# Kernel tuning notes

Hardware: AMD Instinct MI355X
Metric: run time of the kernel (lower is better)

Reference implementation:

```python
import jax, jax.numpy as jnp
import numpy as np

EPS = 1e-12  # F.normalize default eps


def _l2norm(x, axis):
    n = jnp.sqrt(jnp.sum(x * x, axis=axis, keepdims=True))
    return x / jnp.maximum(n, EPS)


def setup_inputs() -> dict:
    key = jax.random.key(0)
    k1, k2, k3, k4 = jax.random.split(key, 4)
    N, T, C, K = 64, 577, 768, 64
    return {
        "grids": jax.random.normal(k1, (N, T, C), dtype=jnp.float32),
        "conv_w": jax.random.normal(k2, (K, C), dtype=jnp.float32) * 0.03,
        "conv_b": jax.random.normal(k3, (K,), dtype=jnp.float32) * 0.01,
        "centroids": jax.random.normal(k4, (K, C), dtype=jnp.float32) * 0.03,
    }


def reference(grids, conv_w, conv_b, centroids):
    # grids: (N, 577, 768) -> (N, C=768, T=577), matching view+permute in torch
    N = grids.shape[0]
    x = jnp.transpose(grids.reshape(N, 577, 768), (0, 2, 1))  # (N, C, T)
    # per-token L2 normalization over channel dim
    x = _l2norm(x, axis=1)
    # 1x1 conv == per-token linear: (N, K, T)
    logits = jnp.einsum('kc,nct->nkt', conv_w, x) + conv_b[None, :, None]
    a = jax.nn.softmax(logits, axis=1)  # softmax over regions K
    # NetVLAD algebraic rewrite of sum_t a[n,k,t]*(x[n,:,t]-c[k,:]):
    #   = (a @ x^T)[n,k,c] - sum_t(a)[n,k] * c[k,c]
    p = jnp.einsum('nkt,nct->nkc', a, x) - a.sum(axis=-1)[:, :, None] * centroids[None]
    p = _l2norm(p, axis=2)             # intra-region normalization
    p = p.reshape(N, -1)               # (N, K*C)
    p = _l2norm(p, axis=1)             # global normalization
    return p
```

## Files before the change

kernel.cpp:

```cpp
#include <hip/hip_runtime.h>
#include <math.h>

#define TT 577
#define TP 640
#define CCH 768
#define KR 64
#define NB 64

typedef __attribute__((ext_vector_type(8))) short bf16x8;
typedef __attribute__((ext_vector_type(8))) unsigned short ushort8;
typedef __attribute__((ext_vector_type(4))) float f32x4;

static constexpr float EPSF = 1e-12f;

static __device__ inline unsigned short f2bf(float f) {
    union { float f; unsigned int u; } v; v.f = f;
    return (unsigned short)((v.u + 0x7FFFu + ((v.u >> 16) & 1u)) >> 16);
}

__global__ __launch_bounds__(256) void k_logits(
    const float* __restrict__ grids,
    const float* __restrict__ conv_w,
    const float* __restrict__ conv_b,
    unsigned short* __restrict__ ws_a,
    float* __restrict__ ws_asum)
{
    __shared__ __align__(16) unsigned short Wl[2][KR * 136];

    const int tid  = threadIdx.x;
    const int lane = tid & 63;
    const int w    = tid >> 6;
    const int n    = blockIdx.x / 10;
    const int tb   = (blockIdx.x - n * 10) << 6;
    const int t0w  = tb + (w << 4);

    const int lr = lane & 15;
    const int lg = lane >> 4;

    const int tokA = t0w + lr;
    const bool validA = (tokA < TT);
    const float* gsrc = grids + ((size_t)n * TT + tokA) * CCH + (lg << 3);

    float4 wreg[4][2];
    auto load_w = [&](int c0) {
        #pragma unroll
        for (int it = 0; it < 4; ++it) {
            int f = tid + (it << 8);
            int kr = f >> 4, c8 = (f & 15) << 3;
            const float* src = conv_w + (size_t)kr * CCH + c0 + c8;
            wreg[it][0] = *reinterpret_cast<const float4*>(src);
            wreg[it][1] = *reinterpret_cast<const float4*>(src + 4);
        }
    };
    auto store_w = [&](int buf) {
        #pragma unroll
        for (int it = 0; it < 4; ++it) {
            int f = tid + (it << 8);
            int kr = f >> 4, c8 = (f & 15) << 3;
            ushort8 o;
            o[0] = f2bf(wreg[it][0].x); o[1] = f2bf(wreg[it][0].y);
            o[2] = f2bf(wreg[it][0].z); o[3] = f2bf(wreg[it][0].w);
            o[4] = f2bf(wreg[it][1].x); o[5] = f2bf(wreg[it][1].y);
            o[6] = f2bf(wreg[it][1].z); o[7] = f2bf(wreg[it][1].w);
            *reinterpret_cast<ushort8*>(&Wl[buf][kr * 136 + c8]) = o;
        }
    };

    f32x4 acc[4] = {};
    float ss = 0.f;

    load_w(0);
    store_w(0);
    __syncthreads();

    for (int ch = 0; ch < 6; ++ch) {
        if (ch < 5) {
            load_w((ch + 1) << 7);
            store_w((ch + 1) & 1);
        }
        const int c0 = ch << 7;
        const unsigned short* Wb = Wl[ch & 1];

        #pragma unroll
        for (int s = 0; s < 4; ++s) {
            float a8[8];
            if (validA) {
                float4 u0 = *reinterpret_cast<const float4*>(gsrc + c0 + (s << 5));
                float4 u1 = *reinterpret_cast<const float4*>(gsrc + c0 + (s << 5) + 4);
                a8[0]=u0.x; a8[1]=u0.y; a8[2]=u0.z; a8[3]=u0.w;
                a8[4]=u1.x; a8[5]=u1.y; a8[6]=u1.z; a8[7]=u1.w;
            } else {
                #pragma unroll
                for (int j = 0; j < 8; ++j) a8[j] = 0.f;
            }
            bf16x8 afrag;
            #pragma unroll
            for (int j = 0; j < 8; ++j) {
                ss = fmaf(a8[j], a8[j], ss);
                ((unsigned short*)&afrag)[j] = f2bf(a8[j]);
            }
            const int cl = (s << 5) + (lg << 3);
            #pragma unroll
            for (int rt = 0; rt < 4; ++rt) {
                bf16x8 bfrag = *reinterpret_cast<const bf16x8*>(&Wb[(rt*16 + lr)*136 + cl]);
                acc[rt] = __builtin_amdgcn_mfma_f32_16x16x32_bf16(afrag, bfrag, acc[rt], 0, 0, 0);
            }
        }
        __syncthreads();
    }

    ss += __shfl_xor(ss, 16);
    ss += __shfl_xor(ss, 32);
    const float nrm = sqrtf(ss);
    const float inv = 1.0f / fmaxf(nrm, EPSF);

    float b_[4];
    #pragma unroll
    for (int rt = 0; rt < 4; ++rt) b_[rt] = conv_b[rt*16 + lr];

    float invT[4];
    #pragma unroll
    for (int reg = 0; reg < 4; ++reg) invT[reg] = __shfl(inv, (lg << 2) + reg);

    float lgt[4][4], mx[4];
    #pragma unroll
    for (int reg = 0; reg < 4; ++reg) {
        float m = -1e30f;
        #pragma unroll
        for (int rt = 0; rt < 4; ++rt) {
            lgt[rt][reg] = fmaf(acc[rt][reg], invT[reg], b_[rt]);
            m = fmaxf(m, lgt[rt][reg]);
        }
        mx[reg] = m;
    }
    #pragma unroll
    for (int msk = 1; msk < 16; msk <<= 1) {
        #pragma unroll
        for (int reg = 0; reg < 4; ++reg) mx[reg] = fmaxf(mx[reg], __shfl_xor(mx[reg], msk));
    }
    float ex[4][4], sm[4] = {0.f, 0.f, 0.f, 0.f};
    #pragma unroll
    for (int rt = 0; rt < 4; ++rt) {
        #pragma unroll
        for (int reg = 0; reg < 4; ++reg) {
            ex[rt][reg] = __expf(lgt[rt][reg] - mx[reg]);
            sm[reg] += ex[rt][reg];
        }
    }
    #pragma unroll
    for (int msk = 1; msk < 16; msk <<= 1) {
        #pragma unroll
        for (int reg = 0; reg < 4; ++reg) sm[reg] += __shfl_xor(sm[reg], msk);
    }

    float rsm[4];
    #pragma unroll
    for (int reg = 0; reg < 4; ++reg) {
        const bool vt = (t0w + (lg << 2) + reg) < TT;
        rsm[reg] = vt ? (1.0f / sm[reg]) : 0.f;
    }

    float pa[4];
    #pragma unroll
    for (int rt = 0; rt < 4; ++rt) {
        pa[rt] = ex[rt][0]*rsm[0] + ex[rt][1]*rsm[1] + ex[rt][2]*rsm[2] + ex[rt][3]*rsm[3];
        pa[rt] += __shfl_xor(pa[rt], 16);
        pa[rt] += __shfl_xor(pa[rt], 32);
    }
    float* asum_lds = reinterpret_cast<float*>(&Wl[1][0]);
    if (lane < 16) {
        #pragma unroll
        for (int rt = 0; rt < 4; ++rt)
            asum_lds[(w << 6) + rt*16 + lane] = pa[rt];
    }

    unsigned short* Abuf = &Wl[0][0] + (size_t)w * KR * 24;
    #pragma unroll
    for (int reg = 0; reg < 4; ++reg) {
        const int trow = (lg << 2) + reg;
        const float scale = invT[reg] * rsm[reg];
        #pragma unroll
        for (int rt = 0; rt < 4; ++rt)
            Abuf[(rt*16 + lr)*24 + trow] = f2bf(ex[rt][reg] * scale);
    }
    __syncthreads();

    if (tid < 64)
        ws_asum[(size_t)blockIdx.x * 64 + tid] =
            asum_lds[tid] + asum_lds[64 + tid] + asum_lds[128 + tid] + asum_lds[192 + tid];

    {
        ushort8 r0 = *reinterpret_cast<const ushort8*>(&Abuf[lane * 24]);
        ushort8 r1 = *reinterpret_cast<const ushort8*>(&Abuf[lane * 24 + 8]);
        unsigned short* dst = ws_a + ((size_t)n * KR + lane) * TP + t0w;
        *reinterpret_cast<ushort8*>(dst)     = r0;
        *reinterpret_cast<ushort8*>(dst + 8) = r1;
    }
}

#define LOADA(d0,d1,d2,d3,t0_)                                                   \
    d0 = *reinterpret_cast<const bf16x8*>(abase +            (size_t)(t0_));     \
    d1 = *reinterpret_cast<const bf16x8*>(abase + 16*TP +    (size_t)(t0_));     \
    d2 = *reinterpret_cast<const bf16x8*>(abase + 32*TP +    (size_t)(t0_));     \
    d3 = *reinterpret_cast<const bf16x8*>(abase + 48*TP +    (size_t)(t0_));

#define LOADB(d,t0_) do {                                                        \
    const int tb2_ = (t0_) + (lg << 3);                                          \
    if ((t0_) + 32 <= TT) {                                                      \
        _Pragma("unroll")                                                        \
        for (int j_ = 0; j_ < 8; ++j_)                                           \
            ((unsigned short*)&(d))[j_] = f2bf(gb[(size_t)(tb2_ + j_) * CCH]);   \
    } else {                                                                     \
        _Pragma("unroll")                                                        \
        for (int j_ = 0; j_ < 8; ++j_) {                                         \
            float v_ = (tb2_ + j_ < TT) ? gb[(size_t)(tb2_ + j_) * CCH] : 0.f;   \
            ((unsigned short*)&(d))[j_] = f2bf(v_);                              \
        }                                                                        \
    } } while (0)

__global__ __launch_bounds__(256) void k_vlad(
    const float* __restrict__ grids,
    const unsigned short* __restrict__ ws_a,
    const float* __restrict__ ws_asum,
    const float* __restrict__ centroids,
    float* __restrict__ out)
{
    __shared__ float asum_s[64];

    const int tid  = threadIdx.x;
    const int lane = tid & 63;
    const int w    = tid >> 6;
    const int n    = blockIdx.x / 12;
    const int c0   = (blockIdx.x - n * 12) << 6;
    const int lr   = lane & 15;
    const int lg   = lane >> 4;

    if (tid < 64) {
        float s = 0.f;
        #pragma unroll
        for (int b = 0; b < 10; ++b)
            s += ws_asum[((size_t)n * 10 + b) * 64 + tid];
        asum_s[tid] = s;
    }
    __syncthreads();

    const int c = c0 + (w << 4) + lr;
    const unsigned short* abase = ws_a + ((size_t)n * KR + lr) * TP + (lg << 3);
    const float* gb = grids + (size_t)n * TT * CCH + c;

    f32x4 acc0 = {}, acc1 = {}, acc2 = {}, acc3 = {};
    bf16x8 a0, a1, a2, a3, b0;
    bf16x8 p0, p1, p2, p3, q0;

    LOADA(a0, a1, a2, a3, 0)
    LOADB(b0, 0);

    int t0 = 0;
    while (true) {
        int tn = t0 + 32;
        if (tn < TT) { LOADA(p0, p1, p2, p3, tn) LOADB(q0, tn); }
        acc0 = __builtin_amdgcn_mfma_f32_16x16x32_bf16(a0, b0, acc0, 0, 0, 0);
        acc1 = __builtin_amdgcn_mfma_f32_16x16x32_bf16(a1, b0, acc1, 0, 0, 0);
        acc2 = __builtin_amdgcn_mfma_f32_16x16x32_bf16(a2, b0, acc2, 0, 0, 0);
        acc3 = __builtin_amdgcn_mfma_f32_16x16x32_bf16(a3, b0, acc3, 0, 0, 0);
        t0 = tn;
        if (t0 >= TT) break;

        tn = t0 + 32;
        if (tn < TT) { LOADA(a0, a1, a2, a3, tn) LOADB(b0, tn); }
        acc0 = __builtin_amdgcn_mfma_f32_16x16x32_bf16(p0, q0, acc0, 0, 0, 0);
        acc1 = __builtin_amdgcn_mfma_f32_16x16x32_bf16(p1, q0, acc1, 0, 0, 0);
        acc2 = __builtin_amdgcn_mfma_f32_16x16x32_bf16(p2, q0, acc2, 0, 0, 0);
        acc3 = __builtin_amdgcn_mfma_f32_16x16x32_bf16(p3, q0, acc3, 0, 0, 0);
        t0 = tn;
        if (t0 >= TT) break;
    }

    #pragma unroll
    for (int reg = 0; reg < 4; ++reg) {
        {
            const int kr = 0*16 + (lg << 2) + reg;
            out[((size_t)n * KR + kr) * CCH + c] =
                acc0[reg] - asum_s[kr] * centroids[(size_t)kr * CCH + c];
        }
        {
            const int kr = 1*16 + (lg << 2) + reg;
            out[((size_t)n * KR + kr) * CCH + c] =
                acc1[reg] - asum_s[kr] * centroids[(size_t)kr * CCH + c];
        }
        {
            const int kr = 2*16 + (lg << 2) + reg;
            out[((size_t)n * KR + kr) * CCH + c] =
                acc2[reg] - asum_s[kr] * centroids[(size_t)kr * CCH + c];
        }
        {
            const int kr = 3*16 + (lg << 2) + reg;
            out[((size_t)n * KR + kr) * CCH + c] =
                acc3[reg] - asum_s[kr] * centroids[(size_t)kr * CCH + c];
        }
    }
}

__global__ __launch_bounds__(64) void kc_norm_kernel(float* __restrict__ out)
{
    float4* p = reinterpret_cast<float4*>(out) + (size_t)blockIdx.x * 192;
    const int l = threadIdx.x;
    float4 v0 = p[l];
    float4 v1 = p[l + 64];
    float4 v2 = p[l + 128];
    float ss = v0.x*v0.x + v0.y*v0.y + v0.z*v0.z + v0.w*v0.w
             + v1.x*v1.x + v1.y*v1.y + v1.z*v1.z + v1.w*v1.w
             + v2.x*v2.x + v2.y*v2.y + v2.z*v2.z + v2.w*v2.w;
    #pragma unroll
    for (int m = 1; m < 64; m <<= 1) ss += __shfl_xor(ss, m);
    const float sc = 0.125f / fmaxf(sqrtf(ss), EPSF);
    v0.x*=sc; v0.y*=sc; v0.z*=sc; v0.w*=sc;
    v1.x*=sc; v1.y*=sc; v1.z*=sc; v1.w*=sc;
    v2.x*=sc; v2.y*=sc; v2.z*=sc; v2.w*=sc;
    p[l] = v0;
    p[l + 64] = v1;
    p[l + 128] = v2;
}

extern "C" void kernel_launch(void* const* d_in, const int* in_sizes, int n_in,
                              void* d_out, int out_size, void* d_ws, size_t ws_size,
                              hipStream_t stream)
{
    const float* grids     = (const float*)d_in[0];
    const float* conv_w    = (const float*)d_in[1];
    const float* conv_b    = (const float*)d_in[2];
    const float* centroids = (const float*)d_in[3];
    float* out = (float*)d_out;

    unsigned short* ws_a = (unsigned short*)d_ws;
    float* ws_asum = (float*)((char*)d_ws + (size_t)NB * KR * TP * 2);

    hipLaunchKernelGGL(k_logits, dim3(NB * 10), dim3(256), 0, stream,
                       grids, conv_w, conv_b, ws_a, ws_asum);
    hipLaunchKernelGGL(k_vlad, dim3(NB * 12), dim3(256), 0, stream,
                       grids, ws_a, ws_asum, centroids, out);
    hipLaunchKernelGGL(kc_norm_kernel, dim3(NB * KR), dim3(64), 0, stream, out);
}
```

Baseline: 73.18 us.

## Emit transposed bf16 tokens from logits kernel and read them in vlad GEMM

The logits kernel now writes the bf16-converted, token-major activations into a transposed workspace buffer (channel-major, padded token dimension) through an LDS staging tile. The vlad kernel then loads contiguous bf16x8 vectors from that buffer instead of gathering strided fp32 grid values and converting them. This removes the uncoalesced strided global reads in the second GEMM, at the cost of writing and reading an extra ~63MB bf16 intermediate. The loop now ends at a padded bound, and the norm kernel uses 256-thread blocks. A counter buffer is zeroed but never used.

```diff
diff --git a/kernel.cpp b/kernel.cpp
--- a/kernel.cpp
+++ b/kernel.cpp
@@ -1,8 +1,10 @@
 #include <hip/hip_runtime.h>
+#include <hip/hip_bf16.h>
 #include <math.h>
 
 #define TT 577
 #define TP 640
+#define TEND 608
 #define CCH 768
 #define KR 64
 #define NB 64
@@ -14,8 +16,7 @@
 static constexpr float EPSF = 1e-12f;
 
 static __device__ inline unsigned short f2bf(float f) {
-    union { float f; unsigned int u; } v; v.f = f;
-    return (unsigned short)((v.u + 0x7FFFu + ((v.u >> 16) & 1u)) >> 16);
+    return __bfloat16_as_ushort(__float2bfloat16(f));
 }
 
 __global__ __launch_bounds__(256) void k_logits(
@@ -23,9 +24,12 @@
     const float* __restrict__ conv_w,
     const float* __restrict__ conv_b,
     unsigned short* __restrict__ ws_a,
-    float* __restrict__ ws_asum)
+    float* __restrict__ ws_asum,
+    unsigned short* __restrict__ ws_x,
+    int* __restrict__ ws_cnt)
 {
     __shared__ __align__(16) unsigned short Wl[2][KR * 136];
+    __shared__ __align__(16) unsigned short Xt[4][64 * 24];
 
     const int tid  = threadIdx.x;
     const int lane = tid & 63;
@@ -33,6 +37,8 @@
     const int n    = blockIdx.x / 10;
     const int tb   = (blockIdx.x - n * 10) << 6;
     const int t0w  = tb + (w << 4);
+
+    if (blockIdx.x == 0 && tid < NB) ws_cnt[tid] = 0;
 
     const int lr = lane & 15;
     const int lg = lane >> 4;
@@ -99,11 +105,28 @@
                 ss = fmaf(a8[j], a8[j], ss);
                 ((unsigned short*)&afrag)[j] = f2bf(a8[j]);
             }
-            const int cl = (s << 5) + (lg << 3);
+            {
+                const int cl = ((s & 1) << 5) + (lg << 3);
+                #pragma unroll
+                for (int j = 0; j < 8; ++j)
+                    Xt[w][(cl + j) * 24 + lr] = ((unsigned short*)&afrag)[j];
+            }
+            const int clW = (s << 5) + (lg << 3);
             #pragma unroll
             for (int rt = 0; rt < 4; ++rt) {
-                bf16x8 bfrag = *reinterpret_cast<const bf16x8*>(&Wb[(rt*16 + lr)*136 + cl]);
+                bf16x8 bfrag = *reinterpret_cast<const bf16x8*>(&Wb[(rt*16 + lr)*136 + clW]);
                 acc[rt] = __builtin_amdgcn_mfma_f32_16x16x32_bf16(afrag, bfrag, acc[rt], 0, 0, 0);
+            }
+            if (s & 1) {
+                const int cbase = c0 + ((s >> 1) << 6);
+                #pragma unroll
+                for (int i = 0; i < 2; ++i) {
+                    const int r = (i << 5) + (lane >> 1);
+                    const int h = lane & 1;
+                    ushort8 v = *reinterpret_cast<const ushort8*>(&Xt[w][r * 24 + (h << 3)]);
+                    *reinterpret_cast<ushort8*>(
+                        ws_x + ((size_t)n * CCH + cbase + r) * TP + t0w + (h << 3)) = v;
+                }
             }
         }
         __syncthreads();
@@ -199,27 +222,16 @@
 }
 
 #define LOADA(d0,d1,d2,d3,t0_)                                                   \
-    d0 = *reinterpret_cast<const bf16x8*>(abase +            (size_t)(t0_));     \
-    d1 = *reinterpret_cast<const bf16x8*>(abase + 16*TP +    (size_t)(t0_));     \
-    d2 = *reinterpret_cast<const bf16x8*>(abase + 32*TP +    (size_t)(t0_));     \
-    d3 = *reinterpret_cast<const bf16x8*>(abase + 48*TP +    (size_t)(t0_));
-
-#define LOADB(d,t0_) do {                                                        \
-    const int tb2_ = (t0_) + (lg << 3);                                          \
-    if ((t0_) + 32 <= TT) {                                                      \
-        _Pragma("unroll")                                                        \
-        for (int j_ = 0; j_ < 8; ++j_)                                           \
-            ((unsigned short*)&(d))[j_] = f2bf(gb[(size_t)(tb2_ + j_) * CCH]);   \
-    } else {                                                                     \
-        _Pragma("unroll")                                                        \
-        for (int j_ = 0; j_ < 8; ++j_) {                                         \
-            float v_ = (tb2_ + j_ < TT) ? gb[(size_t)(tb2_ + j_) * CCH] : 0.f;   \
-            ((unsigned short*)&(d))[j_] = f2bf(v_);                              \
-        }                                                                        \
-    } } while (0)
+    d0 = *reinterpret_cast<const bf16x8*>(abase +           (size_t)(t0_));      \
+    d1 = *reinterpret_cast<const bf16x8*>(abase + 16*TP +   (size_t)(t0_));      \
+    d2 = *reinterpret_cast<const bf16x8*>(abase + 32*TP +   (size_t)(t0_));      \
+    d3 = *reinterpret_cast<const bf16x8*>(abase + 48*TP +   (size_t)(t0_));
+
+#define LOADB(d,t0_)                                                             \
+    d = *reinterpret_cast<const bf16x8*>(xbase + (size_t)(t0_));
 
 __global__ __launch_bounds__(256) void k_vlad(
-    const float* __restrict__ grids,
+    const unsigned short* __restrict__ ws_x,
     const unsigned short* __restrict__ ws_a,
     const float* __restrict__ ws_asum,
     const float* __restrict__ centroids,
@@ -246,34 +258,34 @@
 
     const int c = c0 + (w << 4) + lr;
     const unsigned short* abase = ws_a + ((size_t)n * KR + lr) * TP + (lg << 3);
-    const float* gb = grids + (size_t)n * TT * CCH + c;
+    const unsigned short* xbase = ws_x + ((size_t)n * CCH + c) * TP + (lg << 3);
 
     f32x4 acc0 = {}, acc1 = {}, acc2 = {}, acc3 = {};
     bf16x8 a0, a1, a2, a3, b0;
     bf16x8 p0, p1, p2, p3, q0;
 
     LOADA(a0, a1, a2, a3, 0)
-    LOADB(b0, 0);
+    LOADB(b0, 0)
 
     int t0 = 0;
     while (true) {
         int tn = t0 + 32;
-        if (tn < TT) { LOADA(p0, p1, p2, p3, tn) LOADB(q0, tn); }
+        if (tn < TEND) { LOADA(p0, p1, p2, p3, tn) LOADB(q0, tn) }
         acc0 = __builtin_amdgcn_mfma_f32_16x16x32_bf16(a0, b0, acc0, 0, 0, 0);
         acc1 = __builtin_amdgcn_mfma_f32_16x16x32_bf16(a1, b0, acc1, 0, 0, 0);
         acc2 = __builtin_amdgcn_mfma_f32_16x16x32_bf16(a2, b0, acc2, 0, 0, 0);
         acc3 = __builtin_amdgcn_mfma_f32_16x16x32_bf16(a3, b0, acc3, 0, 0, 0);
         t0 = tn;
-        if (t0 >= TT) break;
+        if (t0 >= TEND) break;
 
         tn = t0 + 32;
-        if (tn < TT) { LOADA(a0, a1, a2, a3, tn) LOADB(b0, tn); }
+        if (tn < TEND) { LOADA(a0, a1, a2, a3, tn) LOADB(b0, tn) }
         acc0 = __builtin_amdgcn_mfma_f32_16x16x32_bf16(p0, q0, acc0, 0, 0, 0);
         acc1 = __builtin_amdgcn_mfma_f32_16x16x32_bf16(p1, q0, acc1, 0, 0, 0);
         acc2 = __builtin_amdgcn_mfma_f32_16x16x32_bf16(p2, q0, acc2, 0, 0, 0);
         acc3 = __builtin_amdgcn_mfma_f32_16x16x32_bf16(p3, q0, acc3, 0, 0, 0);
         t0 = tn;
-        if (t0 >= TT) break;
+        if (t0 >= TEND) break;
     }
 
     #pragma unroll
@@ -301,10 +313,12 @@
     }
 }
 
-__global__ __launch_bounds__(64) void kc_norm_kernel(float* __restrict__ out)
+__global__ __launch_bounds__(256) void kc_norm_kernel(float* __restrict__ out)
 {
-    float4* p = reinterpret_cast<float4*>(out) + (size_t)blockIdx.x * 192;
-    const int l = threadIdx.x;
+    const int tid = threadIdx.x;
+    const int sub = tid >> 6;
+    const int l   = tid & 63;
+    float4* p = reinterpret_cast<float4*>(out) + ((size_t)blockIdx.x * 4 + sub) * 192;
     float4 v0 = p[l];
     float4 v1 = p[l + 64];
     float4 v2 = p[l + 128];
@@ -332,12 +346,14 @@
     const float* centroids = (const float*)d_in[3];
     float* out = (float*)d_out;
 
-    unsigned short* ws_a = (unsigned short*)d_ws;
-    float* ws_asum = (float*)((char*)d_ws + (size_t)NB * KR * TP * 2);
+    unsigned short* ws_a   = (unsigned short*)d_ws;
+    float*          ws_asum= (float*)((char*)d_ws + 5242880);
+    unsigned short* ws_x   = (unsigned short*)((char*)d_ws + 5406720);
+    int*            ws_cnt = (int*)((char*)d_ws + 68301440);
 
     hipLaunchKernelGGL(k_logits, dim3(NB * 10), dim3(256), 0, stream,
-                       grids, conv_w, conv_b, ws_a, ws_asum);
+                       grids, conv_w, conv_b, ws_a, ws_asum, ws_x, ws_cnt);
     hipLaunchKernelGGL(k_vlad, dim3(NB * 12), dim3(256), 0, stream,
-                       grids, ws_a, ws_asum, centroids, out);
-    hipLaunchKernelGGL(kc_norm_kernel, dim3(NB * KR), dim3(64), 0, stream, out);
-}
+                       ws_x, ws_a, ws_asum, centroids, out);
+    hipLaunchKernelGGL(kc_norm_kernel, dim3(NB * KR / 4), dim3(256), 0, stream, out);
+}
```

After: 85.08 us. 16.3% more time.

## Stage full conv weight in LDS once and register-prefetch grid tiles in logits

Applied to the files above, without the earlier changes.

The logits kernel now converts the whole 64x768 conv weight to bf16 into LDS up front instead of double-buffering 128-column chunks with a barrier per chunk. The grid loads are software-pipelined through two register sets of 8 float4 each, so global loads overlap the MFMA steps. The intent is to remove the per-chunk syncs and expose more memory-level parallelism, at the cost of roughly 100KB of LDS per block, which may limit occupancy. The bf16 conversion now uses the library intrinsic, and the per-region norm kernel packs four rows into each 256-thread block.

```diff
diff --git a/kernel.cpp b/kernel.cpp
--- a/kernel.cpp
+++ b/kernel.cpp
@@ -1,11 +1,14 @@
 #include <hip/hip_runtime.h>
+#include <hip/hip_bf16.h>
 #include <math.h>
 
 #define TT 577
 #define TP 640
+#define TEND 608
 #define CCH 768
 #define KR 64
 #define NB 64
+#define WSTR 776
 
 typedef __attribute__((ext_vector_type(8))) short bf16x8;
 typedef __attribute__((ext_vector_type(8))) unsigned short ushort8;
@@ -14,9 +17,48 @@
 static constexpr float EPSF = 1e-12f;
 
 static __device__ inline unsigned short f2bf(float f) {
-    union { float f; unsigned int u; } v; v.f = f;
-    return (unsigned short)((v.u + 0x7FFFu + ((v.u >> 16) & 1u)) >> 16);
-}
+    return __bfloat16_as_ushort(__float2bfloat16(f));
+}
+
+
+#define LOADG(p0,p1,p2,p3,p4,p5,p6,p7, cb)                                     \
+    if (validA) {                                                              \
+        p0 = *reinterpret_cast<const float4*>(gsrc + (cb));                    \
+        p1 = *reinterpret_cast<const float4*>(gsrc + (cb) + 4);                \
+        p2 = *reinterpret_cast<const float4*>(gsrc + (cb) + 32);               \
+        p3 = *reinterpret_cast<const float4*>(gsrc + (cb) + 36);               \
+        p4 = *reinterpret_cast<const float4*>(gsrc + (cb) + 64);               \
+        p5 = *reinterpret_cast<const float4*>(gsrc + (cb) + 68);               \
+        p6 = *reinterpret_cast<const float4*>(gsrc + (cb) + 96);               \
+        p7 = *reinterpret_cast<const float4*>(gsrc + (cb) + 100);              \
+    } else {                                                                   \
+        p0=p1=p2=p3=p4=p5=p6=p7 = make_float4(0.f,0.f,0.f,0.f);                \
+    }
+
+#define STEP(u0,u1, ccol)                                                      \
+    {                                                                          \
+        ss = fmaf(u0.x,u0.x, fmaf(u0.y,u0.y, fmaf(u0.z,u0.z,                   \
+             fmaf(u0.w,u0.w, fmaf(u1.x,u1.x, fmaf(u1.y,u1.y,                   \
+             fmaf(u1.z,u1.z, fmaf(u1.w,u1.w, ss))))))));                       \
+        bf16x8 afrag;                                                          \
+        ((unsigned short*)&afrag)[0] = f2bf(u0.x);                             \
+        ((unsigned short*)&afrag)[1] = f2bf(u0.y);                             \
+        ((unsigned short*)&afrag)[2] = f2bf(u0.z);                             \
+        ((unsigned short*)&afrag)[3] = f2bf(u0.w);                             \
+        ((unsigned short*)&afrag)[4] = f2bf(u1.x);                             \
+        ((unsigned short*)&afrag)[5] = f2bf(u1.y);                             \
+        ((unsigned short*)&afrag)[6] = f2bf(u1.z);                             \
+        ((unsigned short*)&afrag)[7] = f2bf(u1.w);                             \
+        const unsigned short* wp_ = &Wf[(ccol) + (lg << 3) + lr * WSTR];       \
+        bf16x8 bf0_ = *reinterpret_cast<const bf16x8*>(wp_);                   \
+        bf16x8 bf1_ = *reinterpret_cast<const bf16x8*>(wp_ + 16 * WSTR);       \
+        bf16x8 bf2_ = *reinterpret_cast<const bf16x8*>(wp_ + 32 * WSTR);       \
+        bf16x8 bf3_ = *reinterpret_cast<const bf16x8*>(wp_ + 48 * WSTR);       \
+        acc[0] = __builtin_amdgcn_mfma_f32_16x16x32_bf16(afrag, bf0_, acc[0], 0, 0, 0); \
+        acc[1] = __builtin_amdgcn_mfma_f32_16x16x32_bf16(afrag, bf1_, acc[1], 0, 0, 0); \
+        acc[2] = __builtin_amdgcn_mfma_f32_16x16x32_bf16(afrag, bf2_, acc[2], 0, 0, 0); \
+        acc[3] = __builtin_amdgcn_mfma_f32_16x16x32_bf16(afrag, bf3_, acc[3], 0, 0, 0); \
+    }
 
 __global__ __launch_bounds__(256) void k_logits(
     const float* __restrict__ grids,
@@ -25,7 +67,9 @@
     unsigned short* __restrict__ ws_a,
     float* __restrict__ ws_asum)
 {
-    __shared__ __align__(16) unsigned short Wl[2][KR * 136];
+    __shared__ __align__(16) unsigned short Wf[KR * WSTR];
+    __shared__ __align__(16) unsigned short Abuf[4][KR * 24];
+    __shared__ float asum_lds[4][64];
 
     const int tid  = threadIdx.x;
     const int lane = tid & 63;
@@ -41,72 +85,40 @@
     const bool validA = (tokA < TT);
     const float* gsrc = grids + ((size_t)n * TT + tokA) * CCH + (lg << 3);
 
-    float4 wreg[4][2];
-    auto load_w = [&](int c0) {
-        #pragma unroll
-        for (int it = 0; it < 4; ++it) {
-            int f = tid + (it << 8);
-            int kr = f >> 4, c8 = (f & 15) << 3;
-            const float* src = conv_w + (size_t)kr * CCH + c0 + c8;
-            wreg[it][0] = *reinterpret_cast<const float4*>(src);
-            wreg[it][1] = *reinterpret_cast<const float4*>(src + 4);
-        }
-    };
-    auto store_w = [&](int buf) {
-        #pragma unroll
-        for (int it = 0; it < 4; ++it) {
-            int f = tid + (it << 8);
-            int kr = f >> 4, c8 = (f & 15) << 3;
-            ushort8 o;
-            o[0] = f2bf(wreg[it][0].x); o[1] = f2bf(wreg[it][0].y);
-            o[2] = f2bf(wreg[it][0].z); o[3] = f2bf(wreg[it][0].w);
-            o[4] = f2bf(wreg[it][1].x); o[5] = f2bf(wreg[it][1].y);
-            o[6] = f2bf(wreg[it][1].z); o[7] = f2bf(wreg[it][1].w);
-            *reinterpret_cast<ushort8*>(&Wl[buf][kr * 136 + c8]) = o;
-        }
-    };
+    #pragma unroll
+    for (int it = 0; it < 24; ++it) {
+        int f = tid + (it << 8);
+        int kr = f / 96;
+        int c8 = (f - kr * 96) << 3;
+        const float* src = conv_w + (size_t)kr * CCH + c8;
+        float4 v0 = *reinterpret_cast<const float4*>(src);
+        float4 v1 = *reinterpret_cast<const float4*>(src + 4);
+        ushort8 o;
+        o[0]=f2bf(v0.x); o[1]=f2bf(v0.y); o[2]=f2bf(v0.z); o[3]=f2bf(v0.w);
+        o[4]=f2bf(v1.x); o[5]=f2bf(v1.y); o[6]=f2bf(v1.z); o[7]=f2bf(v1.w);
+        *reinterpret_cast<ushort8*>(&Wf[kr * WSTR + c8]) = o;
+    }
+    __syncthreads();
 
     f32x4 acc[4] = {};
     float ss = 0.f;
-
-    load_w(0);
-    store_w(0);
-    __syncthreads();
-
-    for (int ch = 0; ch < 6; ++ch) {
-        if (ch < 5) {
-            load_w((ch + 1) << 7);
-            store_w((ch + 1) & 1);
-        }
-        const int c0 = ch << 7;
-        const unsigned short* Wb = Wl[ch & 1];
-
-        #pragma unroll
-        for (int s = 0; s < 4; ++s) {
-            float a8[8];
-            if (validA) {
-                float4 u0 = *reinterpret_cast<const float4*>(gsrc + c0 + (s << 5));
-                float4 u1 = *reinterpret_cast<const float4*>(gsrc + c0 + (s << 5) + 4);
-                a8[0]=u0.x; a8[1]=u0.y; a8[2]=u0.z; a8[3]=u0.w;
-                a8[4]=u1.x; a8[5]=u1.y; a8[6]=u1.z; a8[7]=u1.w;
-            } else {
-                #pragma unroll
-                for (int j = 0; j < 8; ++j) a8[j] = 0.f;
-            }
-            bf16x8 afrag;
-            #pragma unroll
-            for (int j = 0; j < 8; ++j) {
-                ss = fmaf(a8[j], a8[j], ss);
-                ((unsigned short*)&afrag)[j] = f2bf(a8[j]);
-            }
-            const int cl = (s << 5) + (lg << 3);
-            #pragma unroll
-            for (int rt = 0; rt < 4; ++rt) {
-                bf16x8 bfrag = *reinterpret_cast<const bf16x8*>(&Wb[(rt*16 + lr)*136 + cl]);
-                acc[rt] = __builtin_amdgcn_mfma_f32_16x16x32_bf16(afrag, bfrag, acc[rt], 0, 0, 0);
-            }
-        }
-        __syncthreads();
+    float4 ga0,ga1,ga2,ga3,ga4,ga5,ga6,ga7;
+    float4 gb0,gb1,gb2,gb3,gb4,gb5,gb6,gb7;
+
+    LOADG(ga0,ga1,ga2,ga3,ga4,ga5,ga6,ga7, 0)
+    #pragma unroll
+    for (int cp = 0; cp < 3; ++cp) {
+        const int cb = cp << 8;
+        LOADG(gb0,gb1,gb2,gb3,gb4,gb5,gb6,gb7, cb + 128)
+        STEP(ga0,ga1, cb)
+        STEP(ga2,ga3, cb + 32)
+        STEP(ga4,ga5, cb + 64)
+        STEP(ga6,ga7, cb + 96)
+        if (cp < 2) { LOADG(ga0,ga1,ga2,ga3,ga4,ga5,ga6,ga7, cb + 256) }
+        STEP(gb0,gb1, cb + 128)
+        STEP(gb2,gb3, cb + 160)
+        STEP(gb4,gb5, cb + 192)
+        STEP(gb6,gb7, cb + 224)
     }
 
     ss += __shfl_xor(ss, 16);
@@ -167,31 +179,29 @@
         pa[rt] += __shfl_xor(pa[rt], 16);
         pa[rt] += __shfl_xor(pa[rt], 32);
     }
-    float* asum_lds = reinterpret_cast<float*>(&Wl[1][0]);
     if (lane < 16) {
         #pragma unroll
         for (int rt = 0; rt < 4; ++rt)
-            asum_lds[(w << 6) + rt*16 + lane] = pa[rt];
-    }
-
-    unsigned short* Abuf = &Wl[0][0] + (size_t)w * KR * 24;
+            asum_lds[w][rt*16 + lane] = pa[rt];
+    }
+
     #pragma unroll
     for (int reg = 0; reg < 4; ++reg) {
         const int trow = (lg << 2) + reg;
         const float scale = invT[reg] * rsm[reg];
         #pragma unroll
         for (int rt = 0; rt < 4; ++rt)
-            Abuf[(rt*16 + lr)*24 + trow] = f2bf(ex[rt][reg] * scale);
+            Abuf[w][(rt*16 + lr)*24 + trow] = f2bf(ex[rt][reg] * scale);
     }
     __syncthreads();
 
     if (tid < 64)
         ws_asum[(size_t)blockIdx.x * 64 + tid] =
-            asum_lds[tid] + asum_lds[64 + tid] + asum_lds[128 + tid] + asum_lds[192 + tid];
+            asum_lds[0][tid] + asum_lds[1][tid] + asum_lds[2][tid] + asum_lds[3][tid];
 
     {
-        ushort8 r0 = *reinterpret_cast<const ushort8*>(&Abuf[lane * 24]);
-        ushort8 r1 = *reinterpret_cast<const ushort8*>(&Abuf[lane * 24 + 8]);
+        ushort8 r0 = *reinterpret_cast<const ushort8*>(&Abuf[w][lane * 24]);
+        ushort8 r1 = *reinterpret_cast<const ushort8*>(&Abuf[w][lane * 24 + 8]);
         unsigned short* dst = ws_a + ((size_t)n * KR + lane) * TP + t0w;
         *reinterpret_cast<ushort8*>(dst)     = r0;
         *reinterpret_cast<ushort8*>(dst + 8) = r1;
@@ -199,10 +209,10 @@
 }
 
 #define LOADA(d0,d1,d2,d3,t0_)                                                   \
-    d0 = *reinterpret_cast<const bf16x8*>(abase +            (size_t)(t0_));     \
-    d1 = *reinterpret_cast<const bf16x8*>(abase + 16*TP +    (size_t)(t0_));     \
-    d2 = *reinterpret_cast<const bf16x8*>(abase + 32*TP +    (size_t)(t0_));     \
-    d3 = *reinterpret_cast<const bf16x8*>(abase + 48*TP +    (size_t)(t0_));
+    d0 = *reinterpret_cast<const bf16x8*>(abase +           (size_t)(t0_));      \
+    d1 = *reinterpret_cast<const bf16x8*>(abase + 16*TP +   (size_t)(t0_));      \
+    d2 = *reinterpret_cast<const bf16x8*>(abase + 32*TP +   (size_t)(t0_));      \
+    d3 = *reinterpret_cast<const bf16x8*>(abase + 48*TP +   (size_t)(t0_));
 
 #define LOADB(d,t0_) do {                                                        \
     const int tb2_ = (t0_) + (lg << 3);                                          \
@@ -301,10 +311,12 @@
     }
 }
 
-__global__ __launch_bounds__(64) void kc_norm_kernel(float* __restrict__ out)
+__global__ __launch_bounds__(256) void kc_norm_kernel(float* __restrict__ out)
 {
-    float4* p = reinterpret_cast<float4*>(out) + (size_t)blockIdx.x * 192;
-    const int l = threadIdx.x;
+    const int tid = threadIdx.x;
+    const int sub = tid >> 6;
+    const int l   = tid & 63;
+    float4* p = reinterpret_cast<float4*>(out) + ((size_t)blockIdx.x * 4 + sub) * 192;
     float4 v0 = p[l];
     float4 v1 = p[l + 64];
     float4 v2 = p[l + 128];
@@ -332,12 +344,12 @@
     const float* centroids = (const float*)d_in[3];
     float* out = (float*)d_out;
 
-    unsigned short* ws_a = (unsigned short*)d_ws;
-    float* ws_asum = (float*)((char*)d_ws + (size_t)NB * KR * TP * 2);
+    unsigned short* ws_a    = (unsigned short*)d_ws;
+    float*          ws_asum = (float*)((char*)d_ws + 5242880);
 
     hipLaunchKernelGGL(k_logits, dim3(NB * 10), dim3(256), 0, stream,
                        grids, conv_w, conv_b, ws_a, ws_asum);
     hipLaunchKernelGGL(k_vlad, dim3(NB * 12), dim3(256), 0, stream,
                        grids, ws_a, ws_asum, centroids, out);
-    hipLaunchKernelGGL(kc_norm_kernel, dim3(NB * KR), dim3(64), 0, stream, out);
-}
+    hipLaunchKernelGGL(kc_norm_kernel, dim3(NB * KR / 4), dim3(256), 0, stream, out);
+}
```

After: 80.73 us. +10.3%, slower.
